# Kernel optimization log

Hardware: AMD Instinct MI355X
Metric: run time of the kernel (lower is better)

## Reference

```python
import jax, jax.numpy as jnp
import numpy as np

DELTA = 1.0

def _lin(x, W, b):
    return x @ W + b

def _node(x, child_c, child_h, Wioux, bioux, Wiouh, biouh, Wfx, bfx, Wfh, bfh):
    # Child-sum TreeLSTM cell. x: [B, D]; child_c, child_h: [B, nc, M]
    h_sum = child_h.sum(axis=1)  # [B, M]
    iou = _lin(x, Wioux, bioux) + _lin(h_sum, Wiouh, biouh)  # [B, 3M]
    i, o, u = jnp.split(iou, 3, axis=-1)
    i, o, u = jax.nn.sigmoid(i), jax.nn.sigmoid(o), jnp.tanh(u)
    # forget gate per child: fh(child_h) + fx(x) broadcast over children
    f = jax.nn.sigmoid(_lin(child_h, Wfh, bfh) + _lin(x, Wfx, bfx)[:, None, :])  # [B, nc, M]
    c = i * u + (f * child_c).sum(axis=1)
    h = o * jnp.tanh(c)
    return c, h

def _treelstm(xs, Wioux, bioux, Wiouh, biouh, Wfx, bfx, Wfh, bfh):
    # xs: [B, 4, D]. Fixed 4-node tree: root = node 3, leaf children = {0,1,2}.
    # All leaves (same depth) are batched into one fused gate GEMM.
    B, _, D = xs.shape
    M = Wfx.shape[1]
    gates = (Wioux, bioux, Wiouh, biouh, Wfx, bfx, Wfh, bfh)
    x_leaf = xs[:, :3].reshape(B * 3, D)
    z = jnp.zeros((B * 3, 1, M), xs.dtype)  # leaves get zero child state
    c_l, h_l = _node(x_leaf, z, z, *gates)
    c_root, h_root = _node(xs[:, 3], c_l.reshape(B, 3, M), h_l.reshape(B, 3, M), *gates)
    return c_root, h_root

def setup_inputs() -> dict:
    key = jax.random.key(0)
    B, L, Lq, V, D, M, H, O = 512, 64, 128, 50000, 512, 512, 256, 30
    ks = jax.random.split(key, 24)
    ri = lambda k, shape: jax.random.randint(k, shape, 0, V)
    rn = lambda k, shape, s: jax.random.normal(k, shape, jnp.float32) * s
    return {
        'q_v': ri(ks[0], (B, L)), 'q_a0': ri(ks[1], (B, L)), 'n_a0': ri(ks[2], (B, L)),
        'q_a1': ri(ks[3], (B, L)), 'n_a1': ri(ks[4], (B, L)), 'q_a2': ri(ks[5], (B, L)),
        'n_a2': ri(ks[6], (B, L)),
        'query': ri(ks[7], (B, Lq)), 'pos': ri(ks[8], (B, Lq)), 'neg': ri(ks[9], (B, Lq)),
        'emb': rn(ks[10], (V, D), 0.02),
        'Wioux': rn(ks[11], (D, 3 * M), D ** -0.5), 'bioux': jnp.zeros((3 * M,), jnp.float32),
        'Wiouh': rn(ks[12], (M, 3 * M), M ** -0.5), 'biouh': jnp.zeros((3 * M,), jnp.float32),
        'Wfx': rn(ks[13], (D, M), D ** -0.5), 'bfx': jnp.zeros((M,), jnp.float32),
        'Wfh': rn(ks[14], (M, M), M ** -0.5), 'bfh': jnp.zeros((M,), jnp.float32),
        'Wwh': rn(ks[15], (M, H), M ** -0.5), 'bwh': jnp.zeros((H,), jnp.float32),
        'Wwp': rn(ks[16], (H, O), H ** -0.5), 'bwp': jnp.zeros((O,), jnp.float32),
    }

def reference(q_v, q_a0, n_a0, q_a1, n_a1, q_a2, n_a2, query, pos, neg,
              emb, Wioux, bioux, Wiouh, biouh, Wfx, bfx, Wfh, bfh, Wwh, bwh, Wwp, bwp):
    D = emb.shape[1]
    pool = lambda ids: emb[ids].mean(axis=1)  # embedding lookup + mean over tokens -> [B, D]
    qv = pool(q_v)
    def trip(qa, na):  # attribute-level triplet hinge loss, per batch row
        return jax.nn.relu(DELTA - (qv * pool(qa)).sum(-1) + (qv * pool(na)).sum(-1))
    loss = trip(q_a0, n_a0) + trip(q_a1, n_a1) + trip(q_a2, n_a2)
    def seq(ids):  # [B, Lq] -> 4 mean-pooled node vectors [B, 4, D]
        e = emb[ids]
        return e.reshape(e.shape[0], 4, -1, D).mean(axis=2)
    gates = (Wioux, bioux, Wiouh, biouh, Wfx, bfx, Wfh, bfh)
    qc, _ = _treelstm(seq(query), *gates)
    pc, _ = _treelstm(seq(pos), *gates)
    nc, _ = _treelstm(seq(neg), *gates)
    sim = lambda l, r: _lin(jax.nn.sigmoid(_lin(l * r, Wwh, bwh)), Wwp, bwp)  # Similarity module
    a = sim(qc, pc).sum(-1)
    b = sim(qc, nc).sum(-1)
    return loss + jax.nn.relu(DELTA - a + b)
```

## Files before the change

kernel.cpp:

```cpp
#include <hip/hip_runtime.h>
#include <hip/hip_bf16.h>


typedef __attribute__((ext_vector_type(8))) short short8;
typedef __attribute__((ext_vector_type(4))) float floatx4;
typedef __attribute__((ext_vector_type(2))) float floatx2;

__device__ inline ushort f2bf(float f) {
    unsigned u = __float_as_uint(f);
    u += 0x7fffu + ((u >> 16) & 1u);
    return (ushort)(u >> 16);
}
__device__ inline float bf2f(ushort u) { return __uint_as_float((unsigned)u << 16); }
__device__ inline float sigm(float x) { return 1.0f / (1.0f + expf(-x)); }

#if defined(__has_builtin)
#if __has_builtin(__builtin_amdgcn_cvt_pk_f32_fp8) && __has_builtin(__builtin_amdgcn_cvt_pk_fp8_f32)
#define HW_FP8 1
#endif
#endif

#ifndef HW_FP8
__device__ inline unsigned enc1(float x) {
    float a = fabsf(x);
    unsigned s = (__float_as_uint(x) >> 31) << 7;
    unsigned b = __float_as_uint(a);
    unsigned uexp = b >> 23;
    if (uexp < 121) {
        int m = (int)(a * 512.0f + 0.5f);
        if (m >= 8) return s | 0x08u;
        return s | (unsigned)m;
    }
    b += 0x00080000u;
    unsigned e = b >> 23;
    if (e > 135u) return s | 0x7Eu;
    return s | ((e - 120u) << 3) | ((b >> 20) & 7u);
}
__device__ inline float dec1(unsigned v) {
    unsigned s = (v >> 7) & 1u, e = (v >> 3) & 15u, m = v & 7u;
    float r = e ? __uint_as_float(((e + 120u) << 23) | (m << 20))
                : (float)m * 0.001953125f;
    return s ? -r : r;
}
#endif

__device__ inline unsigned pk4(float a, float b, float c, float d) {
#ifdef HW_FP8
    int v = 0;
    v = __builtin_amdgcn_cvt_pk_fp8_f32(a, b, v, false);
    v = __builtin_amdgcn_cvt_pk_fp8_f32(c, d, v, true);
    return (unsigned)v;
#else
    return enc1(a) | (enc1(b) << 8) | (enc1(c) << 16) | (enc1(d) << 24);
#endif
}
__device__ inline void dec4_add(unsigned v, float* acc) {
#ifdef HW_FP8
    floatx2 p0 = __builtin_amdgcn_cvt_pk_f32_fp8(v, false);
    floatx2 p1 = __builtin_amdgcn_cvt_pk_f32_fp8(v, true);
    acc[0] += p0[0]; acc[1] += p0[1]; acc[2] += p1[0]; acc[3] += p1[1];
#else
    acc[0] += dec1(v & 255u); acc[1] += dec1((v >> 8) & 255u);
    acc[2] += dec1((v >> 16) & 255u); acc[3] += dec1(v >> 24);
#endif
}

#define GLD16(gp, sp)                                                        \
    __builtin_amdgcn_global_load_lds(                                        \
        (const __attribute__((address_space(1))) unsigned int*)(const void*)(gp), \
        (__attribute__((address_space(3))) unsigned int*)(void*)(sp), 16, 0, 0)

#define FP8_SCALE 64.0f

__global__ __launch_bounds__(256) void prep_all_kernel(
    const float* __restrict__ emb, unsigned char* __restrict__ emb8,
    const float* __restrict__ Wioux, const float* __restrict__ Wiouh,
    const float* __restrict__ Wfh, const float* __restrict__ Wfx,
    const float* __restrict__ Wwh, const float* __restrict__ Wwp,
    const float* __restrict__ bwp,
    ushort* __restrict__ Wcat_t, ushort* __restrict__ Wfh_t,
    ushort* __restrict__ Wfx_t, ushort* __restrict__ Wwh_t,
    float* __restrict__ wsum) {
    __shared__ float tt[32][33];
    int blk = blockIdx.x, tid = threadIdx.x;
    if (blk < 12500) {
        size_t i = ((size_t)blk * 256 + tid) * 8;
        float4 a = *(const float4*)(emb + i);
        float4 b = *(const float4*)(emb + i + 4);
        uint2 o;
        o.x = pk4(a.x * FP8_SCALE, a.y * FP8_SCALE, a.z * FP8_SCALE, a.w * FP8_SCALE);
        o.y = pk4(b.x * FP8_SCALE, b.y * FP8_SCALE, b.z * FP8_SCALE, b.w * FP8_SCALE);
        *(uint2*)(emb8 + i) = o;
        return;
    }
    int tx = tid & 31, ty = tid >> 5;
    if (blk < 14036) {
        int idx = blk - 12500;
        int k0 = (idx & 31) * 32, n0 = (idx >> 5) * 32;
#pragma unroll
        for (int r = 0; r < 4; ++r) {
            int k = k0 + ty + r * 8;
            const float* s = (k < 512) ? Wioux + (size_t)k * 1536
                                       : Wiouh + (size_t)(k - 512) * 1536;
            tt[ty + r * 8][tx] = s[n0 + tx];
        }
        __syncthreads();
#pragma unroll
        for (int r = 0; r < 4; ++r)
            Wcat_t[(size_t)(n0 + ty + r * 8) * 1024 + k0 + tx] = f2bf(tt[tx][ty + r * 8]);
        return;
    }
    if (blk < 14676) {
        const float* W; ushort* Wt; int idx, ncols;
        if (blk < 14292)      { idx = blk - 14036; W = Wfh; Wt = Wfh_t; ncols = 512; }
        else if (blk < 14548) { idx = blk - 14292; W = Wfx; Wt = Wfx_t; ncols = 512; }
        else                  { idx = blk - 14548; W = Wwh; Wt = Wwh_t; ncols = 256; }
        int nt_count = ncols >> 5;
        int k0 = (idx / nt_count) * 32, n0 = (idx % nt_count) * 32;
#pragma unroll
        for (int r = 0; r < 4; ++r)
            tt[ty + r * 8][tx] = W[(size_t)(k0 + ty + r * 8) * ncols + n0 + tx];
        __syncthreads();
#pragma unroll
        for (int r = 0; r < 4; ++r)
            Wt[(size_t)(n0 + ty + r * 8) * 512 + k0 + tx] = f2bf(tt[tx][ty + r * 8]);
        return;
    }
    {
        float s = 0.f;
        for (int o = 0; o < 30; ++o) s += Wwp[tid * 30 + o];
        wsum[tid] = s;
        if (tid == 0) {
            float t = 0.f;
            for (int o = 0; o < 30; ++o) t += bwp[o];
            wsum[256] = t;
        }
    }
}

__global__ __launch_bounds__(256) void mega_gather_kernel(
    const int* __restrict__ q_v,
    const int* __restrict__ qa0, const int* __restrict__ na0,
    const int* __restrict__ qa1, const int* __restrict__ na1,
    const int* __restrict__ qa2, const int* __restrict__ na2,
    const int* __restrict__ query, const int* __restrict__ pos, const int* __restrict__ neg,
    const unsigned char* __restrict__ emb8,
    float* __restrict__ pools, ushort* __restrict__ Xleaf, ushort* __restrict__ XR) {
    __shared__ float sm[256][9];
    int tid = threadIdx.x;
    int c = tid & 63, g = tid >> 6;
    float acc[8] = {};
    if (blockIdx.x < 3584) {
        int s = blockIdx.x >> 9, b = blockIdx.x & 511;
        const int* aptr[7] = {q_v, qa0, na0, qa1, na1, qa2, na2};
        const int* ids = aptr[s] + b * 64 + g * 16;
        uint2 v[16];
#pragma unroll
        for (int t = 0; t < 16; ++t)
            v[t] = *(const uint2*)(emb8 + (size_t)ids[t] * 512 + c * 8);
#pragma unroll
        for (int t = 0; t < 16; ++t) { dec4_add(v[t].x, acc); dec4_add(v[t].y, acc + 4); }
#pragma unroll
        for (int k = 0; k < 8; ++k) sm[tid][k] = acc[k];
        __syncthreads();
        if (tid < 64) {
#pragma unroll
            for (int gg = 1; gg < 4; ++gg)
#pragma unroll
                for (int k = 0; k < 8; ++k) acc[k] += sm[tid + gg * 64][k];
            const float sc = 1.0f / (64.0f * FP8_SCALE);
            float* dst = pools + ((size_t)s * 512 + b) * 512 + tid * 8;
            *(float4*)dst = make_float4(acc[0] * sc, acc[1] * sc, acc[2] * sc, acc[3] * sc);
            *(float4*)(dst + 4) = make_float4(acc[4] * sc, acc[5] * sc, acc[6] * sc, acc[7] * sc);
        }
    } else {
        int idx = blockIdx.x - 3584;
        int t = idx >> 11, rem = idx & 2047, b = rem >> 2, node = rem & 3;
        const int* sptr[3] = {query, pos, neg};
        const int* ids = sptr[t] + b * 128 + node * 32 + g * 8;
        uint2 v[8];
#pragma unroll
        for (int k = 0; k < 8; ++k)
            v[k] = *(const uint2*)(emb8 + (size_t)ids[k] * 512 + c * 8);
#pragma unroll
        for (int k = 0; k < 8; ++k) { dec4_add(v[k].x, acc); dec4_add(v[k].y, acc + 4); }
#pragma unroll
        for (int k = 0; k < 8; ++k) sm[tid][k] = acc[k];
        __syncthreads();
        if (tid < 64) {
#pragma unroll
            for (int gg = 1; gg < 4; ++gg)
#pragma unroll
                for (int k = 0; k < 8; ++k) acc[k] += sm[tid + gg * 64][k];
            const float sc = 1.0f / (32.0f * FP8_SCALE);
            short8 o;
#pragma unroll
            for (int k = 0; k < 8; ++k) o[k] = (short)f2bf(acc[k] * sc);
            if (node < 3) {
                size_t r = ((size_t)(t * 512 + b)) * 3 + node;
                *(short8*)(Xleaf + r * 512 + tid * 8) = o;
            } else {
                size_t r = (size_t)(t * 512 + b);
                *(short8*)(XR + r * 1024 + tid * 8) = o;
            }
        }
    }
}

__device__ inline void cstore(float* C, size_t idx, float v)  { C[idx] = v; }
__device__ inline void cstore(ushort* C, size_t idx, float v) { C[idx] = f2bf(v); }

template <typename OutT>
__device__ __forceinline__ void gemm_body(const ushort* __restrict__ A, int lda,
                                          const ushort* __restrict__ Bt, int ldb,
                                          OutT* __restrict__ C, int ldc, int K,
                                          int bx, int by, ushort* sA, ushort* sB) {
    int tid = threadIdx.x;
    int m0 = bx * 128, n0 = by * 128;
    int w = tid >> 6, lane = tid & 63;
    int wm = (w >> 1) * 64, wn = (w & 1) * 64;
    int l15 = lane & 15, g = lane >> 4;
    int srow = tid >> 2;
    int csw = (((tid & 3) ^ ((tid >> 3) & 3))) * 8;
    int crd = (g ^ ((l15 >> 1) & 3)) * 8;

    const ushort* Ag0 = A + (size_t)(m0 + srow) * lda + csw;
    const ushort* Ag1 = A + (size_t)(m0 + srow + 64) * lda + csw;
    const ushort* Bg0 = Bt + (size_t)(n0 + srow) * ldb + csw;
    const ushort* Bg1 = Bt + (size_t)(n0 + srow + 64) * ldb + csw;

    floatx4 acc[4][4] = {};

    auto stage = [&](int buf, int kb) {
        ushort* dA = sA + buf * 4096;
        ushort* dB = sB + buf * 4096;
        GLD16(Ag0 + kb, dA + w * 512);
        GLD16(Ag1 + kb, dA + 2048 + w * 512);
        GLD16(Bg0 + kb, dB + w * 512);
        GLD16(Bg1 + kb, dB + 2048 + w * 512);
    };

    stage(0, 0);
    __syncthreads();
    int cur = 0;
    for (int kb = 0; kb < K; kb += 32) {
        if (kb + 32 < K) stage(cur ^ 1, kb + 32);
        const ushort* bA = sA + cur * 4096;
        const ushort* bB = sB + cur * 4096;
        short8 af[4], bf[4];
#pragma unroll
        for (int f = 0; f < 4; ++f) {
            af[f] = *(const short8*)(bA + (wm + f * 16 + l15) * 32 + crd);
            bf[f] = *(const short8*)(bB + (wn + f * 16 + l15) * 32 + crd);
        }
#pragma unroll
        for (int i = 0; i < 4; ++i)
#pragma unroll
            for (int j = 0; j < 4; ++j)
                acc[i][j] = __builtin_amdgcn_mfma_f32_16x16x32_bf16(af[i], bf[j], acc[i][j], 0, 0, 0);
        __syncthreads();
        cur ^= 1;
    }
#pragma unroll
    for (int i = 0; i < 4; ++i)
#pragma unroll
        for (int j = 0; j < 4; ++j) {
            int row = m0 + wm + i * 16 + g * 4;
            int col = n0 + wn + j * 16 + l15;
#pragma unroll
            for (int r = 0; r < 4; ++r)
                cstore(C, (size_t)(row + r) * ldc + col, acc[i][j][r]);
        }
}

__global__ __launch_bounds__(256) void g1_dots_kernel(
    const ushort* __restrict__ Xleaf, const ushort* __restrict__ Wcat_t,
    ushort* __restrict__ IOU_l,
    const float* __restrict__ pools, float* __restrict__ lossv) {
    __shared__ alignas(16) ushort sA[8192];
    __shared__ alignas(16) ushort sB[8192];
    __shared__ float red[6][4];
    int blk = blockIdx.x, tid = threadIdx.x;
    if (blk < 432) {
        gemm_body(Xleaf, 512, Wcat_t, 1024, IOU_l, 1536, 512, blk % 36, blk / 36, sA, sB);
        return;
    }
    int b = blk - 432;
    const float* pq = pools + (size_t)b * 512;
    float q0 = pq[tid], q1 = pq[tid + 256];
    float d[6];
#pragma unroll
    for (int a = 0; a < 6; ++a) {
        const float* pa = pools + ((size_t)(a + 1) * 512 + b) * 512;
        d[a] = q0 * pa[tid] + q1 * pa[tid + 256];
    }
    int lane = tid & 63, wid = tid >> 6;
#pragma unroll
    for (int a = 0; a < 6; ++a) {
        float v = d[a];
        for (int off = 32; off; off >>= 1) v += __shfl_down(v, off);
        if (lane == 0) red[a][wid] = v;
    }
    __syncthreads();
    if (tid == 0) {
        float l = 0.f;
#pragma unroll
        for (int i = 0; i < 3; ++i) {
            float dq = red[2*i][0] + red[2*i][1] + red[2*i][2] + red[2*i][3];
            float dn = red[2*i+1][0] + red[2*i+1][1] + red[2*i+1][2] + red[2*i+1][3];
            l += fmaxf(0.f, 1.f - dq + dn);
        }
        lossv[b] = l;
    }
}

__global__ __launch_bounds__(256) void gemm3_kernel(
    const ushort* __restrict__ h_l, const ushort* __restrict__ XR,
    const ushort* __restrict__ Wfh_t, const ushort* __restrict__ Wfx_t,
    const ushort* __restrict__ Wcat_t,
    ushort* __restrict__ FH, ushort* __restrict__ FX, ushort* __restrict__ IOU_r) {
    __shared__ alignas(16) ushort sA[8192];
    __shared__ alignas(16) ushort sB[8192];
    int r = blockIdx.x;
    if (r < 144)      gemm_body(XR, 1024, Wcat_t, 1024, IOU_r, 1536, 1024, r % 12, r / 12, sA, sB);
    else if (r < 288) { int q = r - 144; gemm_body(h_l, 512, Wfh_t, 512, FH, 512, 512, q % 36, q / 36, sA, sB); }
    else              { int q = r - 288; gemm_body(XR, 1024, Wfx_t, 512, FX, 512, 512, q % 12, q / 12, sA, sB); }
}

__global__ __launch_bounds__(256) void gemm_sim_kernel(
    const float* __restrict__ c_root, const ushort* __restrict__ Wwh_t,
    float* __restrict__ S) {
    __shared__ alignas(16) ushort sA[8192];
    __shared__ alignas(16) ushort sB[8192];
    int tid = threadIdx.x;
    int bx = blockIdx.x & 7, by = blockIdx.x >> 3;
    int m0 = bx * 128, n0 = by * 128;
    int w = tid >> 6, lane = tid & 63;
    int wm = (w >> 1) * 64, wn = (w & 1) * 64;
    int l15 = lane & 15, g = lane >> 4;
    int srow = tid >> 2;
    int csw = (((tid & 3) ^ ((tid >> 3) & 3))) * 8;
    int crd = (g ^ ((l15 >> 1) & 3)) * 8;

    const ushort* Bg0 = Wwh_t + (size_t)(n0 + srow) * 512 + csw;
    const ushort* Bg1 = Wwh_t + (size_t)(n0 + srow + 64) * 512 + csw;

    floatx4 acc[4][4] = {};

    auto stage = [&](int buf, int kb) {
        ushort* dA = sA + buf * 4096;
        ushort* dB = sB + buf * 4096;
        GLD16(Bg0 + kb, dB + w * 512);
        GLD16(Bg1 + kb, dB + 2048 + w * 512);
#pragma unroll
        for (int half = 0; half < 2; ++half) {
            int gr = m0 + srow + half * 64;
            int b = gr & 511, which = gr >> 9;
            const float* qrow = c_root + (size_t)b * 512 + kb + csw;
            const float* orow = c_root + ((size_t)(which + 1) * 512 + b) * 512 + kb + csw;
            float4 q0 = *(const float4*)qrow, q1 = *(const float4*)(qrow + 4);
            float4 o0 = *(const float4*)orow, o1 = *(const float4*)(orow + 4);
            short8 pv;
            pv[0] = (short)f2bf(q0.x * o0.x); pv[1] = (short)f2bf(q0.y * o0.y);
            pv[2] = (short)f2bf(q0.z * o0.z); pv[3] = (short)f2bf(q0.w * o0.w);
            pv[4] = (short)f2bf(q1.x * o1.x); pv[5] = (short)f2bf(q1.y * o1.y);
            pv[6] = (short)f2bf(q1.z * o1.z); pv[7] = (short)f2bf(q1.w * o1.w);
            *(short8*)(dA + (srow + half * 64) * 32 + (tid & 3) * 8) = pv;
        }
    };

    stage(0, 0);
    __syncthreads();
    int cur = 0;
    for (int kb = 0; kb < 512; kb += 32) {
        if (kb + 32 < 512) stage(cur ^ 1, kb + 32);
        const ushort* bA = sA + cur * 4096;
        const ushort* bB = sB + cur * 4096;
        short8 af[4], bf[4];
#pragma unroll
        for (int f = 0; f < 4; ++f) {
            af[f] = *(const short8*)(bA + (wm + f * 16 + l15) * 32 + crd);
            bf[f] = *(const short8*)(bB + (wn + f * 16 + l15) * 32 + crd);
        }
#pragma unroll
        for (int i = 0; i < 4; ++i)
#pragma unroll
            for (int j = 0; j < 4; ++j)
                acc[i][j] = __builtin_amdgcn_mfma_f32_16x16x32_bf16(af[i], bf[j], acc[i][j], 0, 0, 0);
        __syncthreads();
        cur ^= 1;
    }
#pragma unroll
    for (int i = 0; i < 4; ++i)
#pragma unroll
        for (int j = 0; j < 4; ++j) {
            int row = m0 + wm + i * 16 + g * 4;
            int col = n0 + wn + j * 16 + l15;
#pragma unroll
            for (int r = 0; r < 4; ++r)
                S[(size_t)(row + r) * 256 + col] = acc[i][j][r];
        }
}


__global__ __launch_bounds__(256) void leaf_act_kernel(
    const ushort* __restrict__ IOU_l, const float* __restrict__ bioux,
    const float* __restrict__ biouh, ushort* __restrict__ c_l,
    ushort* __restrict__ h_l, ushort* __restrict__ XR) {
    int tb = blockIdx.x, tid = threadIdx.x;
#pragma unroll
    for (int half = 0; half < 2; ++half) {
        int m = tid + half * 256;
        float bi = bioux[m] + biouh[m];
        float bo = bioux[m + 512] + biouh[m + 512];
        float bu = bioux[m + 1024] + biouh[m + 1024];
        float hs = 0.f;
#pragma unroll
        for (int leaf = 0; leaf < 3; ++leaf) {
            size_t r = (size_t)tb * 3 + leaf;
            const ushort* row = IOU_l + r * 1536;
            float iv = sigm(bf2f(row[m]) + bi);
            float ov = sigm(bf2f(row[m + 512]) + bo);
            float uv = tanhf(bf2f(row[m + 1024]) + bu);
            float c = iv * uv;
            c_l[r * 512 + m] = f2bf(c);
            float h = ov * tanhf(c);
            h_l[r * 512 + m] = f2bf(h);
            hs += h;
        }
        XR[(size_t)tb * 1024 + 512 + m] = f2bf(hs);
    }
}

__global__ __launch_bounds__(256) void root_act_kernel(
    const ushort* __restrict__ IOU_r, const ushort* __restrict__ FH,
    const ushort* __restrict__ FX, const ushort* __restrict__ c_l,
    const float* __restrict__ bioux, const float* __restrict__ biouh,
    const float* __restrict__ bfx, const float* __restrict__ bfh,
    float* __restrict__ c_root) {
    int r = blockIdx.x, tid = threadIdx.x;
#pragma unroll
    for (int half = 0; half < 2; ++half) {
        int m = tid + half * 256;
        float iv = sigm(bf2f(IOU_r[(size_t)r * 1536 + m]) + bioux[m] + biouh[m]);
        float uv = tanhf(bf2f(IOU_r[(size_t)r * 1536 + 1024 + m]) + bioux[1024 + m] + biouh[1024 + m]);
        float fx = bf2f(FX[(size_t)r * 512 + m]) + bfx[m];
        float c = iv * uv;
#pragma unroll
        for (int k = 0; k < 3; ++k) {
            size_t idx = ((size_t)r * 3 + k) * 512 + m;
            float f = sigm(bf2f(FH[idx]) + bfh[m] + fx);
            c += f * bf2f(c_l[idx]);
        }
        c_root[(size_t)r * 512 + m] = c;
    }
}

__global__ __launch_bounds__(256) void final_kernel(
    const float* __restrict__ S, const float* __restrict__ bwh,
    const float* __restrict__ wsum, const float* __restrict__ loss,
    float* __restrict__ out) {
    int b = blockIdx.x, tid = threadIdx.x;
    float w = wsum[tid];
    float bw = bwh[tid];
    float va = sigm(S[(size_t)b * 256 + tid] + bw) * w;
    float vb = sigm(S[(size_t)(512 + b) * 256 + tid] + bw) * w;
    int lane = tid & 63, wid = tid >> 6;
    for (int off = 32; off; off >>= 1) {
        va += __shfl_down(va, off);
        vb += __shfl_down(vb, off);
    }
    __shared__ float ra[4], rb[4];
    if (lane == 0) { ra[wid] = va; rb[wid] = vb; }
    __syncthreads();
    if (tid == 0) {
        float a  = ra[0] + ra[1] + ra[2] + ra[3] + wsum[256];
        float bb = rb[0] + rb[1] + rb[2] + rb[3] + wsum[256];
        out[b] = loss[b] + fmaxf(0.f, 1.f - a + bb);
    }
}


extern "C" void kernel_launch(void* const* d_in, const int* in_sizes, int n_in,
                              void* d_out, int out_size, void* d_ws, size_t ws_size,
                              hipStream_t stream) {
    const int* q_v   = (const int*)d_in[0];
    const int* q_a0  = (const int*)d_in[1];
    const int* n_a0  = (const int*)d_in[2];
    const int* q_a1  = (const int*)d_in[3];
    const int* n_a1  = (const int*)d_in[4];
    const int* q_a2  = (const int*)d_in[5];
    const int* n_a2  = (const int*)d_in[6];
    const int* query = (const int*)d_in[7];
    const int* pos   = (const int*)d_in[8];
    const int* neg   = (const int*)d_in[9];
    const float* emb   = (const float*)d_in[10];
    const float* Wioux = (const float*)d_in[11];
    const float* bioux = (const float*)d_in[12];
    const float* Wiouh = (const float*)d_in[13];
    const float* biouh = (const float*)d_in[14];
    const float* Wfx   = (const float*)d_in[15];
    const float* bfx   = (const float*)d_in[16];
    const float* Wfh   = (const float*)d_in[17];
    const float* bfh   = (const float*)d_in[18];
    const float* Wwh   = (const float*)d_in[19];
    const float* bwh   = (const float*)d_in[20];
    const float* Wwp   = (const float*)d_in[21];
    const float* bwp   = (const float*)d_in[22];
    float* out = (float*)d_out;

    char* w = (char*)d_ws;
    size_t off = 0;
    auto alloc = [&](size_t bytes) -> void* {
        void* p = (void*)(w + off);
        off = (off + bytes + 255) & ~(size_t)255;
        return p;
    };
    ushort* Wcat_t = (ushort*)alloc((size_t)1536 * 1024 * 2);
    ushort* Wfh_t  = (ushort*)alloc((size_t)512 * 512 * 2);
    ushort* Wfx_t  = (ushort*)alloc((size_t)512 * 512 * 2);
    ushort* Wwh_t  = (ushort*)alloc((size_t)256 * 512 * 2);
    float*  wsum   = (float*) alloc(257 * 4);
    float*  lossv  = (float*) alloc(512 * 4);
    ushort* Xleaf  = (ushort*)alloc((size_t)4608 * 512 * 2);
    ushort* XR     = (ushort*)alloc((size_t)1536 * 1024 * 2);
    size_t xbase = off;
    unsigned char* emb8 = (unsigned char*)alloc((size_t)50000 * 512);
    float* pools        = (float*)        alloc((size_t)7 * 512 * 512 * 4);
    off = xbase;
    ushort* IOU_l  = (ushort*)alloc((size_t)4608 * 1536 * 2);
    ushort* c_l    = (ushort*)alloc((size_t)4608 * 512 * 2);
    ushort* h_l    = (ushort*)alloc((size_t)4608 * 512 * 2);
    ushort* FH     = (ushort*)alloc((size_t)4608 * 512 * 2);
    ushort* FX     = (ushort*)alloc((size_t)1536 * 512 * 2);
    ushort* IOU_r  = (ushort*)alloc((size_t)1536 * 1536 * 2);
    float*  c_root = (float*) alloc((size_t)1536 * 512 * 4);
    float*  S      = (float*) alloc((size_t)1024 * 256 * 4);

    prep_all_kernel<<<14677, 256, 0, stream>>>(emb, emb8, Wioux, Wiouh, Wfh, Wfx, Wwh,
                                               Wwp, bwp, Wcat_t, Wfh_t, Wfx_t, Wwh_t, wsum);
    mega_gather_kernel<<<9728, 256, 0, stream>>>(q_v, q_a0, n_a0, q_a1, n_a1, q_a2, n_a2,
                                                 query, pos, neg, emb8, pools, Xleaf, XR);
    g1_dots_kernel<<<944, 256, 0, stream>>>(Xleaf, Wcat_t, IOU_l, pools, lossv);
    leaf_act_kernel<<<1536, 256, 0, stream>>>(IOU_l, bioux, biouh, c_l, h_l, XR);
    gemm3_kernel<<<336, 256, 0, stream>>>(h_l, XR, Wfh_t, Wfx_t, Wcat_t, FH, FX, IOU_r);
    root_act_kernel<<<1536, 256, 0, stream>>>(IOU_r, FH, FX, c_l, bioux, biouh, bfx, bfh, c_root);
    gemm_sim_kernel<<<16, 256, 0, stream>>>(c_root, Wwh_t, S);
    final_kernel<<<512, 256, 0, stream>>>(S, bwh, wsum, lossv, out);
}
```

Measured before the change: 123.5 us.

## Regroup prep kernels and vectorize gather and activation kernels

The embedding fp8 conversion now runs in its own kernel with 16 floats per thread. The weight-transpose blocks move into the gather kernel, so the independent weight prep overlaps with the embedding gather. The gather uses 16-byte loads per thread, with 32 column-chunks and 8 token groups reduced through shared memory. The leaf and root activation kernels now process 8 contiguous elements per thread with short8/float4 vector loads and stores, and four rows per block instead of one, which cuts the number of memory transactions and blocks.

```diff
diff --git a/kernel.cpp b/kernel.cpp
--- a/kernel.cpp
+++ b/kernel.cpp
@@ -72,8 +72,29 @@
 
 #define FP8_SCALE 64.0f
 
-__global__ __launch_bounds__(256) void prep_all_kernel(
-    const float* __restrict__ emb, unsigned char* __restrict__ emb8,
+__global__ __launch_bounds__(256) void conv_kernel(const float* __restrict__ emb,
+                                                   unsigned char* __restrict__ emb8) {
+    size_t i = ((size_t)blockIdx.x * 256 + threadIdx.x) * 16;
+    float4 a = *(const float4*)(emb + i);
+    float4 b = *(const float4*)(emb + i + 4);
+    float4 c = *(const float4*)(emb + i + 8);
+    float4 d = *(const float4*)(emb + i + 12);
+    uint4 o;
+    o.x = pk4(a.x * FP8_SCALE, a.y * FP8_SCALE, a.z * FP8_SCALE, a.w * FP8_SCALE);
+    o.y = pk4(b.x * FP8_SCALE, b.y * FP8_SCALE, b.z * FP8_SCALE, b.w * FP8_SCALE);
+    o.z = pk4(c.x * FP8_SCALE, c.y * FP8_SCALE, c.z * FP8_SCALE, c.w * FP8_SCALE);
+    o.w = pk4(d.x * FP8_SCALE, d.y * FP8_SCALE, d.z * FP8_SCALE, d.w * FP8_SCALE);
+    *(uint4*)(emb8 + i) = o;
+}
+
+__global__ __launch_bounds__(256) void gather_wprep_kernel(
+    const int* __restrict__ q_v,
+    const int* __restrict__ qa0, const int* __restrict__ na0,
+    const int* __restrict__ qa1, const int* __restrict__ na1,
+    const int* __restrict__ qa2, const int* __restrict__ na2,
+    const int* __restrict__ query, const int* __restrict__ pos, const int* __restrict__ neg,
+    const unsigned char* __restrict__ emb8,
+    float* __restrict__ pools, ushort* __restrict__ Xleaf, ushort* __restrict__ XR,
     const float* __restrict__ Wioux, const float* __restrict__ Wiouh,
     const float* __restrict__ Wfh, const float* __restrict__ Wfx,
     const float* __restrict__ Wwh, const float* __restrict__ Wwp,
@@ -81,49 +102,117 @@
     ushort* __restrict__ Wcat_t, ushort* __restrict__ Wfh_t,
     ushort* __restrict__ Wfx_t, ushort* __restrict__ Wwh_t,
     float* __restrict__ wsum) {
-    __shared__ float tt[32][33];
+    __shared__ alignas(16) char smem_u[16384];
     int blk = blockIdx.x, tid = threadIdx.x;
-    if (blk < 12500) {
-        size_t i = ((size_t)blk * 256 + tid) * 8;
-        float4 a = *(const float4*)(emb + i);
-        float4 b = *(const float4*)(emb + i + 4);
-        uint2 o;
-        o.x = pk4(a.x * FP8_SCALE, a.y * FP8_SCALE, a.z * FP8_SCALE, a.w * FP8_SCALE);
-        o.y = pk4(b.x * FP8_SCALE, b.y * FP8_SCALE, b.z * FP8_SCALE, b.w * FP8_SCALE);
-        *(uint2*)(emb8 + i) = o;
+
+    if (blk < 9728) {
+        float* sm = (float*)smem_u;
+        int c = tid & 31, g = tid >> 5;
+        float acc[16] = {};
+        if (blk < 3584) {
+            int s = blk >> 9, b = blk & 511;
+            const int* aptr[7] = {q_v, qa0, na0, qa1, na1, qa2, na2};
+            const int* ids = aptr[s] + b * 64 + g * 8;
+            uint4 v[8];
+#pragma unroll
+            for (int k = 0; k < 8; ++k)
+                v[k] = *(const uint4*)(emb8 + (size_t)ids[k] * 512 + c * 16);
+#pragma unroll
+            for (int k = 0; k < 8; ++k) {
+                dec4_add(v[k].x, acc); dec4_add(v[k].y, acc + 4);
+                dec4_add(v[k].z, acc + 8); dec4_add(v[k].w, acc + 12);
+            }
+#pragma unroll
+            for (int j = 0; j < 4; ++j)
+                *(float4*)(sm + tid * 16 + j * 4) = *(float4*)(acc + j * 4);
+            __syncthreads();
+            if (tid < 32) {
+#pragma unroll
+                for (int gg = 1; gg < 8; ++gg)
+#pragma unroll
+                    for (int j = 0; j < 16; ++j) acc[j] += sm[(gg * 32 + tid) * 16 + j];
+                const float sc = 1.0f / (64.0f * FP8_SCALE);
+                float* dst = pools + ((size_t)s * 512 + b) * 512 + tid * 16;
+#pragma unroll
+                for (int j = 0; j < 4; ++j)
+                    *(float4*)(dst + j * 4) = make_float4(acc[j*4] * sc, acc[j*4+1] * sc,
+                                                          acc[j*4+2] * sc, acc[j*4+3] * sc);
+            }
+        } else {
+            int idx = blk - 3584;
+            int t = idx >> 11, rem = idx & 2047, b = rem >> 2, node = rem & 3;
+            const int* sptr[3] = {query, pos, neg};
+            const int* ids = sptr[t] + b * 128 + node * 32 + g * 4;
+            uint4 v[4];
+#pragma unroll
+            for (int k = 0; k < 4; ++k)
+                v[k] = *(const uint4*)(emb8 + (size_t)ids[k] * 512 + c * 16);
+#pragma unroll
+            for (int k = 0; k < 4; ++k) {
+                dec4_add(v[k].x, acc); dec4_add(v[k].y, acc + 4);
+                dec4_add(v[k].z, acc + 8); dec4_add(v[k].w, acc + 12);
+            }
+#pragma unroll
+            for (int j = 0; j < 4; ++j)
+                *(float4*)(sm + tid * 16 + j * 4) = *(float4*)(acc + j * 4);
+            __syncthreads();
+            if (tid < 32) {
+#pragma unroll
+                for (int gg = 1; gg < 8; ++gg)
+#pragma unroll
+                    for (int j = 0; j < 16; ++j) acc[j] += sm[(gg * 32 + tid) * 16 + j];
+                const float sc = 1.0f / (32.0f * FP8_SCALE);
+                short8 o0, o1;
+#pragma unroll
+                for (int j = 0; j < 8; ++j) {
+                    o0[j] = (short)f2bf(acc[j] * sc);
+                    o1[j] = (short)f2bf(acc[j + 8] * sc);
+                }
+                if (node < 3) {
+                    size_t r = ((size_t)(t * 512 + b)) * 3 + node;
+                    *(short8*)(Xleaf + r * 512 + tid * 16) = o0;
+                    *(short8*)(Xleaf + r * 512 + tid * 16 + 8) = o1;
+                } else {
+                    size_t r = (size_t)(t * 512 + b);
+                    *(short8*)(XR + r * 1024 + tid * 16) = o0;
+                    *(short8*)(XR + r * 1024 + tid * 16 + 8) = o1;
+                }
+            }
+        }
         return;
     }
+    float* tt = (float*)smem_u;
+    int wblk = blk - 9728;
     int tx = tid & 31, ty = tid >> 5;
-    if (blk < 14036) {
-        int idx = blk - 12500;
-        int k0 = (idx & 31) * 32, n0 = (idx >> 5) * 32;
+    if (wblk < 1536) {
+        int k0 = (wblk & 31) * 32, n0 = (wblk >> 5) * 32;
 #pragma unroll
         for (int r = 0; r < 4; ++r) {
             int k = k0 + ty + r * 8;
             const float* s = (k < 512) ? Wioux + (size_t)k * 1536
                                        : Wiouh + (size_t)(k - 512) * 1536;
-            tt[ty + r * 8][tx] = s[n0 + tx];
+            tt[(ty + r * 8) * 33 + tx] = s[n0 + tx];
         }
         __syncthreads();
 #pragma unroll
         for (int r = 0; r < 4; ++r)
-            Wcat_t[(size_t)(n0 + ty + r * 8) * 1024 + k0 + tx] = f2bf(tt[tx][ty + r * 8]);
+            Wcat_t[(size_t)(n0 + ty + r * 8) * 1024 + k0 + tx] = f2bf(tt[tx * 33 + ty + r * 8]);
         return;
     }
-    if (blk < 14676) {
+    if (wblk < 2176) {
         const float* W; ushort* Wt; int idx, ncols;
-        if (blk < 14292)      { idx = blk - 14036; W = Wfh; Wt = Wfh_t; ncols = 512; }
-        else if (blk < 14548) { idx = blk - 14292; W = Wfx; Wt = Wfx_t; ncols = 512; }
-        else                  { idx = blk - 14548; W = Wwh; Wt = Wwh_t; ncols = 256; }
+        if (wblk < 1792)      { idx = wblk - 1536; W = Wfh; Wt = Wfh_t; ncols = 512; }
+        else if (wblk < 2048) { idx = wblk - 1792; W = Wfx; Wt = Wfx_t; ncols = 512; }
+        else                  { idx = wblk - 2048; W = Wwh; Wt = Wwh_t; ncols = 256; }
         int nt_count = ncols >> 5;
         int k0 = (idx / nt_count) * 32, n0 = (idx % nt_count) * 32;
 #pragma unroll
         for (int r = 0; r < 4; ++r)
-            tt[ty + r * 8][tx] = W[(size_t)(k0 + ty + r * 8) * ncols + n0 + tx];
+            tt[(ty + r * 8) * 33 + tx] = W[(size_t)(k0 + ty + r * 8) * ncols + n0 + tx];
         __syncthreads();
 #pragma unroll
         for (int r = 0; r < 4; ++r)
-            Wt[(size_t)(n0 + ty + r * 8) * 512 + k0 + tx] = f2bf(tt[tx][ty + r * 8]);
+            Wt[(size_t)(n0 + ty + r * 8) * 512 + k0 + tx] = f2bf(tt[tx * 33 + ty + r * 8]);
         return;
     }
     {
@@ -134,75 +223,6 @@
             float t = 0.f;
             for (int o = 0; o < 30; ++o) t += bwp[o];
             wsum[256] = t;
-        }
-    }
-}
-
-__global__ __launch_bounds__(256) void mega_gather_kernel(
-    const int* __restrict__ q_v,
-    const int* __restrict__ qa0, const int* __restrict__ na0,
-    const int* __restrict__ qa1, const int* __restrict__ na1,
-    const int* __restrict__ qa2, const int* __restrict__ na2,
-    const int* __restrict__ query, const int* __restrict__ pos, const int* __restrict__ neg,
-    const unsigned char* __restrict__ emb8,
-    float* __restrict__ pools, ushort* __restrict__ Xleaf, ushort* __restrict__ XR) {
-    __shared__ float sm[256][9];
-    int tid = threadIdx.x;
-    int c = tid & 63, g = tid >> 6;
-    float acc[8] = {};
-    if (blockIdx.x < 3584) {
-        int s = blockIdx.x >> 9, b = blockIdx.x & 511;
-        const int* aptr[7] = {q_v, qa0, na0, qa1, na1, qa2, na2};
-        const int* ids = aptr[s] + b * 64 + g * 16;
-        uint2 v[16];
-#pragma unroll
-        for (int t = 0; t < 16; ++t)
-            v[t] = *(const uint2*)(emb8 + (size_t)ids[t] * 512 + c * 8);
-#pragma unroll
-        for (int t = 0; t < 16; ++t) { dec4_add(v[t].x, acc); dec4_add(v[t].y, acc + 4); }
-#pragma unroll
-        for (int k = 0; k < 8; ++k) sm[tid][k] = acc[k];
-        __syncthreads();
-        if (tid < 64) {
-#pragma unroll
-            for (int gg = 1; gg < 4; ++gg)
-#pragma unroll
-                for (int k = 0; k < 8; ++k) acc[k] += sm[tid + gg * 64][k];
-            const float sc = 1.0f / (64.0f * FP8_SCALE);
-            float* dst = pools + ((size_t)s * 512 + b) * 512 + tid * 8;
-            *(float4*)dst = make_float4(acc[0] * sc, acc[1] * sc, acc[2] * sc, acc[3] * sc);
-            *(float4*)(dst + 4) = make_float4(acc[4] * sc, acc[5] * sc, acc[6] * sc, acc[7] * sc);
-        }
-    } else {
-        int idx = blockIdx.x - 3584;
-        int t = idx >> 11, rem = idx & 2047, b = rem >> 2, node = rem & 3;
-        const int* sptr[3] = {query, pos, neg};
-        const int* ids = sptr[t] + b * 128 + node * 32 + g * 8;
-        uint2 v[8];
-#pragma unroll
-        for (int k = 0; k < 8; ++k)
-            v[k] = *(const uint2*)(emb8 + (size_t)ids[k] * 512 + c * 8);
-#pragma unroll
-        for (int k = 0; k < 8; ++k) { dec4_add(v[k].x, acc); dec4_add(v[k].y, acc + 4); }
-#pragma unroll
-        for (int k = 0; k < 8; ++k) sm[tid][k] = acc[k];
-        __syncthreads();
-        if (tid < 64) {
-#pragma unroll
-            for (int gg = 1; gg < 4; ++gg)
-#pragma unroll
-                for (int k = 0; k < 8; ++k) acc[k] += sm[tid + gg * 64][k];
-            const float sc = 1.0f / (32.0f * FP8_SCALE);
-            short8 o;
-#pragma unroll
-            for (int k = 0; k < 8; ++k) o[k] = (short)f2bf(acc[k] * sc);
-            if (node < 3) {
-                size_t r = ((size_t)(t * 512 + b)) * 3 + node;
-                *(short8*)(Xleaf + r * 512 + tid * 8) = o;
-            } else {
-                size_t r = (size_t)(t * 512 + b);
-                *(short8*)(XR + r * 1024 + tid * 8) = o;
-            }
         }
     }
 }
@@ -407,29 +427,44 @@
     const ushort* __restrict__ IOU_l, const float* __restrict__ bioux,
     const float* __restrict__ biouh, ushort* __restrict__ c_l,
     ushort* __restrict__ h_l, ushort* __restrict__ XR) {
-    int tb = blockIdx.x, tid = threadIdx.x;
-#pragma unroll
-    for (int half = 0; half < 2; ++half) {
-        int m = tid + half * 256;
-        float bi = bioux[m] + biouh[m];
-        float bo = bioux[m + 512] + biouh[m + 512];
-        float bu = bioux[m + 1024] + biouh[m + 1024];
-        float hs = 0.f;
-#pragma unroll
-        for (int leaf = 0; leaf < 3; ++leaf) {
-            size_t r = (size_t)tb * 3 + leaf;
-            const ushort* row = IOU_l + r * 1536;
-            float iv = sigm(bf2f(row[m]) + bi);
-            float ov = sigm(bf2f(row[m + 512]) + bo);
-            float uv = tanhf(bf2f(row[m + 1024]) + bu);
-            float c = iv * uv;
-            c_l[r * 512 + m] = f2bf(c);
-            float h = ov * tanhf(c);
-            h_l[r * 512 + m] = f2bf(h);
-            hs += h;
-        }
-        XR[(size_t)tb * 1024 + 512 + m] = f2bf(hs);
-    }
+    int tb = blockIdx.x * 4 + (threadIdx.x >> 6);
+    int d0 = (threadIdx.x & 63) * 8;
+    float bi[8], bo[8], bu[8];
+#pragma unroll
+    for (int gate = 0; gate < 3; ++gate) {
+        float* dst = gate == 0 ? bi : (gate == 1 ? bo : bu);
+        int m = gate * 512 + d0;
+        float4 x0 = *(const float4*)(bioux + m), x1 = *(const float4*)(bioux + m + 4);
+        float4 h0 = *(const float4*)(biouh + m), h1 = *(const float4*)(biouh + m + 4);
+        dst[0] = x0.x + h0.x; dst[1] = x0.y + h0.y; dst[2] = x0.z + h0.z; dst[3] = x0.w + h0.w;
+        dst[4] = x1.x + h1.x; dst[5] = x1.y + h1.y; dst[6] = x1.z + h1.z; dst[7] = x1.w + h1.w;
+    }
+    float hs[8] = {};
+#pragma unroll
+    for (int leaf = 0; leaf < 3; ++leaf) {
+        size_t r = (size_t)tb * 3 + leaf;
+        short8 vi = *(const short8*)(IOU_l + r * 1536 + d0);
+        short8 vo = *(const short8*)(IOU_l + r * 1536 + 512 + d0);
+        short8 vu = *(const short8*)(IOU_l + r * 1536 + 1024 + d0);
+        short8 cb, hb;
+#pragma unroll
+        for (int j = 0; j < 8; ++j) {
+            float iv = sigm(bf2f((ushort)vi[j]) + bi[j]);
+            float ov = sigm(bf2f((ushort)vo[j]) + bo[j]);
+            float uv = tanhf(bf2f((ushort)vu[j]) + bu[j]);
+            float cc = iv * uv;
+            cb[j] = (short)f2bf(cc);
+            float hh = ov * tanhf(cc);
+            hb[j] = (short)f2bf(hh);
+            hs[j] += hh;
+        }
+        *(short8*)(c_l + r * 512 + d0) = cb;
+        *(short8*)(h_l + r * 512 + d0) = hb;
+    }
+    short8 hsb;
+#pragma unroll
+    for (int j = 0; j < 8; ++j) hsb[j] = (short)f2bf(hs[j]);
+    *(short8*)(XR + (size_t)tb * 1024 + 512 + d0) = hsb;
 }
 
 __global__ __launch_bounds__(256) void root_act_kernel(
@@ -438,22 +473,49 @@
     const float* __restrict__ bioux, const float* __restrict__ biouh,
     const float* __restrict__ bfx, const float* __restrict__ bfh,
     float* __restrict__ c_root) {
-    int r = blockIdx.x, tid = threadIdx.x;
-#pragma unroll
-    for (int half = 0; half < 2; ++half) {
-        int m = tid + half * 256;
-        float iv = sigm(bf2f(IOU_r[(size_t)r * 1536 + m]) + bioux[m] + biouh[m]);
-        float uv = tanhf(bf2f(IOU_r[(size_t)r * 1536 + 1024 + m]) + bioux[1024 + m] + biouh[1024 + m]);
-        float fx = bf2f(FX[(size_t)r * 512 + m]) + bfx[m];
-        float c = iv * uv;
-#pragma unroll
-        for (int k = 0; k < 3; ++k) {
-            size_t idx = ((size_t)r * 3 + k) * 512 + m;
-            float f = sigm(bf2f(FH[idx]) + bfh[m] + fx);
-            c += f * bf2f(c_l[idx]);
-        }
-        c_root[(size_t)r * 512 + m] = c;
-    }
+    int r = blockIdx.x * 4 + (threadIdx.x >> 6);
+    int d0 = (threadIdx.x & 63) * 8;
+    float bi[8], bu[8], bfxv[8], bfhv[8];
+    {
+        float4 x0 = *(const float4*)(bioux + d0), x1 = *(const float4*)(bioux + d0 + 4);
+        float4 h0 = *(const float4*)(biouh + d0), h1 = *(const float4*)(biouh + d0 + 4);
+        bi[0] = x0.x + h0.x; bi[1] = x0.y + h0.y; bi[2] = x0.z + h0.z; bi[3] = x0.w + h0.w;
+        bi[4] = x1.x + h1.x; bi[5] = x1.y + h1.y; bi[6] = x1.z + h1.z; bi[7] = x1.w + h1.w;
+        float4 u0 = *(const float4*)(bioux + 1024 + d0), u1 = *(const float4*)(bioux + 1024 + d0 + 4);
+        float4 v0 = *(const float4*)(biouh + 1024 + d0), v1 = *(const float4*)(biouh + 1024 + d0 + 4);
+        bu[0] = u0.x + v0.x; bu[1] = u0.y + v0.y; bu[2] = u0.z + v0.z; bu[3] = u0.w + v0.w;
+        bu[4] = u1.x + v1.x; bu[5] = u1.y + v1.y; bu[6] = u1.z + v1.z; bu[7] = u1.w + v1.w;
+        float4 f0 = *(const float4*)(bfx + d0), f1 = *(const float4*)(bfx + d0 + 4);
+        bfxv[0] = f0.x; bfxv[1] = f0.y; bfxv[2] = f0.z; bfxv[3] = f0.w;
+        bfxv[4] = f1.x; bfxv[5] = f1.y; bfxv[6] = f1.z; bfxv[7] = f1.w;
+        float4 g0 = *(const float4*)(bfh + d0), g1 = *(const float4*)(bfh + d0 + 4);
+        bfhv[0] = g0.x; bfhv[1] = g0.y; bfhv[2] = g0.z; bfhv[3] = g0.w;
+        bfhv[4] = g1.x; bfhv[5] = g1.y; bfhv[6] = g1.z; bfhv[7] = g1.w;
+    }
+    short8 vi = *(const short8*)(IOU_r + (size_t)r * 1536 + d0);
+    short8 vu = *(const short8*)(IOU_r + (size_t)r * 1536 + 1024 + d0);
+    short8 vfx = *(const short8*)(FX + (size_t)r * 512 + d0);
+    float c[8], fx[8];
+#pragma unroll
+    for (int j = 0; j < 8; ++j) {
+        float iv = sigm(bf2f((ushort)vi[j]) + bi[j]);
+        float uv = tanhf(bf2f((ushort)vu[j]) + bu[j]);
+        fx[j] = bf2f((ushort)vfx[j]) + bfxv[j];
+        c[j] = iv * uv;
+    }
+#pragma unroll
+    for (int k = 0; k < 3; ++k) {
+        size_t rr = ((size_t)r * 3 + k) * 512 + d0;
+        short8 vfh = *(const short8*)(FH + rr);
+        short8 vcl = *(const short8*)(c_l + rr);
+#pragma unroll
+        for (int j = 0; j < 8; ++j) {
+            float f = sigm(bf2f((ushort)vfh[j]) + bfhv[j] + fx[j]);
+            c[j] += f * bf2f((ushort)vcl[j]);
+        }
+    }
+    *(float4*)(c_root + (size_t)r * 512 + d0)     = make_float4(c[0], c[1], c[2], c[3]);
+    *(float4*)(c_root + (size_t)r * 512 + d0 + 4) = make_float4(c[4], c[5], c[6], c[7]);
 }
 
 __global__ __launch_bounds__(256) void final_kernel(
@@ -537,14 +599,15 @@
     float*  c_root = (float*) alloc((size_t)1536 * 512 * 4);
     float*  S      = (float*) alloc((size_t)1024 * 256 * 4);
 
-    prep_all_kernel<<<14677, 256, 0, stream>>>(emb, emb8, Wioux, Wiouh, Wfh, Wfx, Wwh,
-                                               Wwp, bwp, Wcat_t, Wfh_t, Wfx_t, Wwh_t, wsum);
-    mega_gather_kernel<<<9728, 256, 0, stream>>>(q_v, q_a0, n_a0, q_a1, n_a1, q_a2, n_a2,
-                                                 query, pos, neg, emb8, pools, Xleaf, XR);
+    conv_kernel<<<6250, 256, 0, stream>>>(emb, emb8);
+    gather_wprep_kernel<<<11905, 256, 0, stream>>>(q_v, q_a0, n_a0, q_a1, n_a1, q_a2, n_a2,
+                                                   query, pos, neg, emb8, pools, Xleaf, XR,
+                                                   Wioux, Wiouh, Wfh, Wfx, Wwh, Wwp, bwp,
+                                                   Wcat_t, Wfh_t, Wfx_t, Wwh_t, wsum);
     g1_dots_kernel<<<944, 256, 0, stream>>>(Xleaf, Wcat_t, IOU_l, pools, lossv);
-    leaf_act_kernel<<<1536, 256, 0, stream>>>(IOU_l, bioux, biouh, c_l, h_l, XR);
+    leaf_act_kernel<<<384, 256, 0, stream>>>(IOU_l, bioux, biouh, c_l, h_l, XR);
     gemm3_kernel<<<336, 256, 0, stream>>>(h_l, XR, Wfh_t, Wfx_t, Wcat_t, FH, FX, IOU_r);
-    root_act_kernel<<<1536, 256, 0, stream>>>(IOU_r, FH, FX, c_l, bioux, biouh, bfx, bfh, c_root);
+    root_act_kernel<<<384, 256, 0, stream>>>(IOU_r, FH, FX, c_l, bioux, biouh, bfx, bfh, c_root);
     gemm_sim_kernel<<<16, 256, 0, stream>>>(c_root, Wwh_t, S);
     final_kernel<<<512, 256, 0, stream>>>(S, bwh, wsum, lossv, out);
 }
```

After: 132.8 us. +7.5%, slower.
